# Kernel optimization log

Hardware: AMD Instinct MI355X
Metric: run time of the kernel (lower is better)

The kernel has to match this reference:

```python
import jax, jax.numpy as jnp
import numpy as np

N, E, H, NH = 50000, 500000, 128, 8
DH = H // NH


def _bn(x, g, b, eps=1e-5):
    # BatchNorm1d in training mode: biased batch statistics over the node dim
    mu = x.mean(0)
    var = ((x - mu) ** 2).mean(0)
    return (x - mu) * jax.lax.rsqrt(var + eps) * g + b


def setup_inputs() -> dict:
    key = jax.random.key(0)
    ks = jax.random.split(key, 16)
    W = lambda k, shape: jax.random.normal(k, shape, jnp.float32) * 0.02
    return {
        "h": jax.random.normal(ks[0], (N, H), jnp.float32),
        "eattr": jax.random.normal(ks[1], (E, H), jnp.float32),
        "src": jax.random.randint(ks[2], (E,), 0, N, jnp.int32),
        "dst": jax.random.randint(ks[3], (E,), 0, N, jnp.int32),
        "gin_w1": W(ks[4], (H, H)), "gin_b1": jnp.zeros((H,), jnp.float32),
        "gin_w2": W(ks[5], (H, H)), "gin_b2": jnp.zeros((H,), jnp.float32),
        "wq": W(ks[6], (H, H)), "bq": jnp.zeros((H,), jnp.float32),
        "wk": W(ks[7], (H, H)), "bk": jnp.zeros((H,), jnp.float32),
        "wv": W(ks[8], (H, H)), "bv": jnp.zeros((H,), jnp.float32),
        "nl_g": jnp.ones((H,), jnp.float32), "nl_b": jnp.zeros((H,), jnp.float32),
        "na_g": jnp.ones((H,), jnp.float32), "na_b": jnp.zeros((H,), jnp.float32),
        "no_g": jnp.ones((H,), jnp.float32), "no_b": jnp.zeros((H,), jnp.float32),
        "ffn1_w": W(ks[9], (2 * H, H)), "ffn1_b": jnp.zeros((2 * H,), jnp.float32),
        "ffn2_w": W(ks[10], (H, 2 * H)), "ffn2_b": jnp.zeros((H,), jnp.float32),
    }


def reference(h, eattr, src, dst, gin_w1, gin_b1, gin_w2, gin_b2,
              wq, bq, wk, bk, wv, bv, nl_g, nl_b, na_g, na_b, no_g, no_b,
              ffn1_w, ffn1_b, ffn2_w, ffn2_b):
    h_in = h

    # --- local model: GINEConv (eps=0) ---
    msg = jax.nn.relu(h[src] + eattr)                       # [E,H]
    agg = jax.ops.segment_sum(msg, dst, num_segments=N)     # [N,H]
    z = h + agg                                             # (1+eps)*h + sum
    h_local = jax.nn.relu(z @ gin_w1.T + gin_b1) @ gin_w2.T + gin_b2
    h_local = _bn(h_in + h_local, nl_g, nl_b)               # dropout=0

    # --- global attention: SparseMHA over the edge list ---
    scale = DH ** -0.5
    q = ((h @ wq.T + bq) * scale).reshape(N, NH, DH)
    k = (h @ wk.T + bk).reshape(N, NH, DH)
    v = (h @ wv.T + bv).reshape(N, NH, DH)
    s = jnp.einsum("ehd,ehd->eh", q[src], k[dst])           # per-edge scores [E,NH]
    m = jax.ops.segment_max(s, src, num_segments=N)         # row-wise max [N,NH]
    p = jnp.exp(s - m[src])
    denom = jax.ops.segment_sum(p, src, num_segments=N)     # [N,NH]
    attn = p / denom[src]                                   # sparse row softmax [E,NH]
    out = jax.ops.segment_sum(attn[:, :, None] * v[dst], src, num_segments=N)
    h_attn = out.reshape(N, H)
    h_attn = _bn(h_in + h_attn, na_g, na_b)

    # --- combine + FFN + out norm ---
    hc = h_local + h_attn
    hc = hc + (jax.nn.relu(hc @ ffn1_w.T + ffn1_b) @ ffn2_w.T + ffn2_b)
    hc = _bn(hc, no_g, no_b)
    return (hc, eattr)
```

## Files before the change

### kernel.cpp

```cpp
#include <hip/hip_runtime.h>

#define NN 50000
#define NE 500000
#define HD 128

typedef unsigned short ushort_t;
typedef __bf16 bf16x8 __attribute__((ext_vector_type(8)));
typedef float f32x4 __attribute__((ext_vector_type(4)));
typedef float f32x2 __attribute__((ext_vector_type(2)));

static __device__ __forceinline__ unsigned short f2bf(float f) {
  unsigned int u = __float_as_uint(f);
  unsigned int r = (u + 0x7fffu + ((u >> 16) & 1u)) >> 16;
  return (unsigned short)r;
}
static __device__ __forceinline__ float2 ldbf2(const unsigned short* p) {
  unsigned int u = *reinterpret_cast<const unsigned int*>(p);
  return make_float2(__uint_as_float(u << 16), __uint_as_float(u & 0xffff0000u));
}

__global__ __launch_bounds__(256) void hist_kernel(const int* __restrict__ src, const int* __restrict__ dst,
                                                   int* __restrict__ deg_src, int* __restrict__ deg_dst, int E) {
  int e = blockIdx.x * 256 + threadIdx.x;
  if (e < E) {
    atomicAdd(&deg_dst[dst[e]], 1);
    atomicAdd(&deg_src[src[e]], 1);
  }
}

__global__ __launch_bounds__(1024) void scan_kernel(const int* __restrict__ deg_dst, const int* __restrict__ deg_src,
                                                    int* __restrict__ off_dst, int* __restrict__ cur_dst,
                                                    int* __restrict__ off_src, int* __restrict__ cur_src, int N) {
  const int* deg = blockIdx.x ? deg_src : deg_dst;
  int* off = blockIdx.x ? off_src : off_dst;
  int* cur = blockIdx.x ? cur_src : cur_dst;
  const int CH = (N + 1023) / 1024;
  int t = threadIdx.x;
  int base = t * CH;
  int sum = 0;
  for (int i = 0; i < CH; ++i) { int idx = base + i; if (idx < N) sum += deg[idx]; }
  __shared__ int ls[1024];
  ls[t] = sum;
  __syncthreads();
  for (int o = 1; o < 1024; o <<= 1) {
    int u = (t >= o) ? ls[t - o] : 0;
    __syncthreads();
    ls[t] += u;
    __syncthreads();
  }
  int run = ls[t] - sum;
  for (int i = 0; i < CH; ++i) {
    int idx = base + i;
    if (idx < N) { off[idx] = run; cur[idx] = run; run += deg[idx]; }
  }
  if (t == 1023) off[N] = ls[1023];
}

__global__ __launch_bounds__(256) void scatter_kernel(const int* __restrict__ src, const int* __restrict__ dst,
                                                      int* __restrict__ cur_src, int* __restrict__ cur_dst,
                                                      int* __restrict__ adj_src, int2* __restrict__ pair_dst, int E) {
  int e = blockIdx.x * 256 + threadIdx.x;
  if (e < E) {
    int s = src[e], d = dst[e];
    int p = atomicAdd(&cur_dst[d], 1); pair_dst[p] = make_int2(e, s);
    int q = atomicAdd(&cur_src[s], 1); adj_src[q] = d;
  }
}

__global__ __launch_bounds__(256) void hconv_kernel(const float* __restrict__ h, ushort_t* __restrict__ hb, int total4) {
  int i = blockIdx.x * 256 + threadIdx.x;
  if (i >= total4) return;
  float4 v = reinterpret_cast<const float4*>(h)[i];
  ushort4 u = { f2bf(v.x), f2bf(v.y), f2bf(v.z), f2bf(v.w) };
  reinterpret_cast<ushort4*>(hb)[i] = u;
}

template <int K, int OUTC, int MODE>
__global__ __launch_bounds__(256) void gemm_kernel(const ushort_t* __restrict__ A, const float* __restrict__ W,
                                                   const float* __restrict__ bias, const float* __restrict__ resid,
                                                   void* __restrict__ out, float scale, int nrows) {
  constexpr int KP = K + 8;
  __shared__ __align__(16) ushort_t wlds[OUTC * KP];
  constexpr int NLOAD = OUTC * K / 4;
  for (int idx = threadIdx.x; idx < NLOAD; idx += 256) {
    int r = idx / (K / 4), c4 = idx % (K / 4);
    float4 wv = reinterpret_cast<const float4*>(W)[idx];
    ushort_t* d = &wlds[r * KP + c4 * 4];
    d[0] = f2bf(wv.x); d[1] = f2bf(wv.y); d[2] = f2bf(wv.z); d[3] = f2bf(wv.w);
  }
  __syncthreads();
  const int wave = threadIdx.x >> 6, lane = threadIdx.x & 63;
  const int row0 = (blockIdx.x * 4 + wave) * 16;
  if (row0 >= nrows) return;
  const int m = lane & 15, quad = lane >> 4;
  bf16x8 afrag[K / 32];
  {
    const ushort_t* ar = A + (size_t)(row0 + m) * K + quad * 8;
#pragma unroll
    for (int kk = 0; kk < K / 32; ++kk)
      afrag[kk] = *reinterpret_cast<const bf16x8*>(ar + kk * 32);
  }
  f32x4 acc[OUTC / 16] = {};
#pragma unroll
  for (int c = 0; c < OUTC / 16; ++c) {
    const ushort_t* wr = &wlds[(c * 16 + m) * KP + quad * 8];
#pragma unroll
    for (int kk = 0; kk < K / 32; ++kk) {
      bf16x8 bfrag = *reinterpret_cast<const bf16x8*>(wr + kk * 32);
      acc[c] = __builtin_amdgcn_mfma_f32_16x16x32_bf16(afrag[kk], bfrag, acc[c], 0, 0, 0);
    }
  }
#pragma unroll
  for (int c = 0; c < OUTC / 16; ++c) {
    int col = c * 16 + m;
    float bv = bias[col];
#pragma unroll
    for (int r = 0; r < 4; ++r) {
      int grow = row0 + quad * 4 + r;
      float val = (acc[c][r] + bv) * scale;
      if constexpr (MODE & 1) val = fmaxf(val, 0.0f);
      if constexpr (MODE & 2) val += resid[(size_t)grow * OUTC + col];
      if constexpr (MODE & 4) ((ushort_t*)out)[(size_t)grow * OUTC + col] = f2bf(val);
      else ((float*)out)[(size_t)grow * OUTC + col] = val;
    }
  }
}

__global__ __launch_bounds__(256) void agg_kernel(const float* __restrict__ h, const float* __restrict__ eattr,
                                                  const int* __restrict__ off_dst, const int2* __restrict__ pair_dst,
                                                  float* __restrict__ out_eattr, ushort_t* __restrict__ z_bf, int N) {
  int wave = threadIdx.x >> 6, lane = threadIdx.x & 63;
  int n = blockIdx.x * 4 + wave;
  if (n >= N) return;
  int c2 = lane * 2;
  float a0 = 0.f, a1 = 0.f;
  int beg = off_dst[n], end = off_dst[n + 1];
  int i = beg;
  int mainend = beg + ((end - beg) & ~3);
  if (i < mainend) {
    int2 p0 = pair_dst[i], p1 = pair_dst[i + 1], p2 = pair_dst[i + 2], p3 = pair_dst[i + 3];
    for (;;) {
      f32x2 ea0 = __builtin_nontemporal_load(reinterpret_cast<const f32x2*>(eattr + (size_t)p0.x * HD + c2));
      f32x2 ea1 = __builtin_nontemporal_load(reinterpret_cast<const f32x2*>(eattr + (size_t)p1.x * HD + c2));
      f32x2 ea2 = __builtin_nontemporal_load(reinterpret_cast<const f32x2*>(eattr + (size_t)p2.x * HD + c2));
      f32x2 ea3 = __builtin_nontemporal_load(reinterpret_cast<const f32x2*>(eattr + (size_t)p3.x * HD + c2));
      f32x2 hs0 = *reinterpret_cast<const f32x2*>(h + (size_t)p0.y * HD + c2);
      f32x2 hs1 = *reinterpret_cast<const f32x2*>(h + (size_t)p1.y * HD + c2);
      f32x2 hs2 = *reinterpret_cast<const f32x2*>(h + (size_t)p2.y * HD + c2);
      f32x2 hs3 = *reinterpret_cast<const f32x2*>(h + (size_t)p3.y * HD + c2);
      int ni = i + 4;
      int pi = (ni < mainend) ? ni : beg;
      int2 q0 = pair_dst[pi], q1 = pair_dst[pi + 1], q2 = pair_dst[pi + 2], q3 = pair_dst[pi + 3];
      __builtin_nontemporal_store(ea0, reinterpret_cast<f32x2*>(out_eattr + (size_t)p0.x * HD + c2));
      __builtin_nontemporal_store(ea1, reinterpret_cast<f32x2*>(out_eattr + (size_t)p1.x * HD + c2));
      __builtin_nontemporal_store(ea2, reinterpret_cast<f32x2*>(out_eattr + (size_t)p2.x * HD + c2));
      __builtin_nontemporal_store(ea3, reinterpret_cast<f32x2*>(out_eattr + (size_t)p3.x * HD + c2));
      a0 += (fmaxf(hs0.x + ea0.x, 0.f) + fmaxf(hs1.x + ea1.x, 0.f)) +
            (fmaxf(hs2.x + ea2.x, 0.f) + fmaxf(hs3.x + ea3.x, 0.f));
      a1 += (fmaxf(hs0.y + ea0.y, 0.f) + fmaxf(hs1.y + ea1.y, 0.f)) +
            (fmaxf(hs2.y + ea2.y, 0.f) + fmaxf(hs3.y + ea3.y, 0.f));
      p0 = q0; p1 = q1; p2 = q2; p3 = q3;
      i = ni;
      if (i >= mainend) break;
    }
  }
  for (; i < end; ++i) {
    int2 p = pair_dst[i];
    f32x2 ea = __builtin_nontemporal_load(reinterpret_cast<const f32x2*>(eattr + (size_t)p.x * HD + c2));
    f32x2 hs = *reinterpret_cast<const f32x2*>(h + (size_t)p.y * HD + c2);
    __builtin_nontemporal_store(ea, reinterpret_cast<f32x2*>(out_eattr + (size_t)p.x * HD + c2));
    a0 += fmaxf(hs.x + ea.x, 0.f);
    a1 += fmaxf(hs.y + ea.y, 0.f);
  }
  float2 hn = *reinterpret_cast<const float2*>(h + (size_t)n * HD + c2);
  ushort2 u = { f2bf(hn.x + a0), f2bf(hn.y + a1) };
  *reinterpret_cast<ushort2*>(z_bf + (size_t)n * HD + c2) = u;
}

__global__ __launch_bounds__(256) void attn_kernel(const ushort_t* __restrict__ qb, const ushort_t* __restrict__ kb,
                                                   const ushort_t* __restrict__ vb, const int* __restrict__ off_src,
                                                   const int* __restrict__ adj_src,
                                                   const float* __restrict__ h, float* __restrict__ X2, int N) {
  int wave = threadIdx.x >> 6, lane = threadIdx.x & 63;
  int n = blockIdx.x * 4 + wave;
  if (n >= N) return;
  int c2 = lane * 2;
  float2 qv = ldbf2(qb + (size_t)n * HD + c2);
  float m = -__builtin_inff(), l = 0.f, a0 = 0.f, a1 = 0.f;
  int beg = off_src[n], end = off_src[n + 1];
  int i = beg;
  int mainend = beg + ((end - beg) & ~3);
  if (i < mainend) {
    int d0 = adj_src[i], d1 = adj_src[i + 1], d2 = adj_src[i + 2], d3 = adj_src[i + 3];
    for (;;) {
      float2 k0 = ldbf2(kb + (size_t)d0 * HD + c2);
      float2 k1 = ldbf2(kb + (size_t)d1 * HD + c2);
      float2 k2 = ldbf2(kb + (size_t)d2 * HD + c2);
      float2 k3 = ldbf2(kb + (size_t)d3 * HD + c2);
      float2 v0 = ldbf2(vb + (size_t)d0 * HD + c2);
      float2 v1 = ldbf2(vb + (size_t)d1 * HD + c2);
      float2 v2 = ldbf2(vb + (size_t)d2 * HD + c2);
      float2 v3 = ldbf2(vb + (size_t)d3 * HD + c2);
      int ni = i + 4;
      int pi = (ni < mainend) ? ni : beg;
      int e0 = adj_src[pi], e1 = adj_src[pi + 1], e2 = adj_src[pi + 2], e3 = adj_src[pi + 3];
      float s0 = qv.x * k0.x + qv.y * k0.y;
      float s1 = qv.x * k1.x + qv.y * k1.y;
      float s2 = qv.x * k2.x + qv.y * k2.y;
      float s3 = qv.x * k3.x + qv.y * k3.y;
      s0 += __shfl_xor(s0, 1, 64); s0 += __shfl_xor(s0, 2, 64); s0 += __shfl_xor(s0, 4, 64);
      s1 += __shfl_xor(s1, 1, 64); s1 += __shfl_xor(s1, 2, 64); s1 += __shfl_xor(s1, 4, 64);
      s2 += __shfl_xor(s2, 1, 64); s2 += __shfl_xor(s2, 2, 64); s2 += __shfl_xor(s2, 4, 64);
      s3 += __shfl_xor(s3, 1, 64); s3 += __shfl_xor(s3, 2, 64); s3 += __shfl_xor(s3, 4, 64);
      float smax = fmaxf(fmaxf(s0, s1), fmaxf(s2, s3));
      float nm = fmaxf(m, smax);
      float al = __expf(m - nm);
      float p0 = __expf(s0 - nm), p1 = __expf(s1 - nm), p2 = __expf(s2 - nm), p3 = __expf(s3 - nm);
      l = l * al + ((p0 + p1) + (p2 + p3));
      a0 = a0 * al + ((p0 * v0.x + p1 * v1.x) + (p2 * v2.x + p3 * v3.x));
      a1 = a1 * al + ((p0 * v0.y + p1 * v1.y) + (p2 * v2.y + p3 * v3.y));
      m = nm;
      d0 = e0; d1 = e1; d2 = e2; d3 = e3;
      i = ni;
      if (i >= mainend) break;
    }
  }
  for (; i < end; ++i) {
    int d = adj_src[i];
    float2 kd = ldbf2(kb + (size_t)d * HD + c2);
    float s = qv.x * kd.x + qv.y * kd.y;
    s += __shfl_xor(s, 1, 64);
    s += __shfl_xor(s, 2, 64);
    s += __shfl_xor(s, 4, 64);
    float2 vd = ldbf2(vb + (size_t)d * HD + c2);
    float nm = fmaxf(m, s);
    float al = __expf(m - nm);
    float p = __expf(s - nm);
    l = l * al + p;
    a0 = a0 * al + p * vd.x;
    a1 = a1 * al + p * vd.y;
    m = nm;
  }
  float inv = (end > beg) ? 1.0f / l : 0.f;
  size_t base = (size_t)n * HD + c2;
  float2 hv = *reinterpret_cast<const float2*>(h + base);
  float2 o = make_float2(hv.x + a0 * inv, hv.y + a1 * inv);
  *reinterpret_cast<float2*>(X2 + base) = o;
}

__global__ __launch_bounds__(256) void stats_kernel(const float* __restrict__ X, float* __restrict__ sums,
                                                    float* __restrict__ sumsq, int N) {
  int col = threadIdx.x & 127, half = threadIdx.x >> 7;
  float s = 0.f, s2 = 0.f;
  for (int r = blockIdx.x * 2 + half; r < N; r += gridDim.x * 2) {
    float v = X[(size_t)r * HD + col];
    s += v;
    s2 += v * v;
  }
  __shared__ float ls[256], ls2[256];
  ls[threadIdx.x] = s;
  ls2[threadIdx.x] = s2;
  __syncthreads();
  if (half == 0) {
    s += ls[threadIdx.x + 128];
    s2 += ls2[threadIdx.x + 128];
    atomicAdd(&sums[col], s);
    atomicAdd(&sumsq[col], s2);
  }
}

__global__ void coeff_kernel(const float* __restrict__ sums, const float* __restrict__ sumsq,
                             const float* __restrict__ g, const float* __restrict__ b, float* __restrict__ ab, int N) {
  int c = threadIdx.x;
  float inv_n = 1.0f / (float)N;
  float mu = sums[c] * inv_n;
  float var = sumsq[c] * inv_n - mu * mu;
  float a = g[c] * rsqrtf(var + 1e-5f);
  ab[c] = a;
  ab[128 + c] = b[c] - mu * a;
}

__global__ __launch_bounds__(256) void combine_kernel(const float* __restrict__ X1, const float* __restrict__ X2,
                                                      const float* __restrict__ ab1, const float* __restrict__ ab2,
                                                      float* __restrict__ hc_f, ushort_t* __restrict__ hc_b, int total4) {
  int i = blockIdx.x * 256 + threadIdx.x;
  if (i >= total4) return;
  float4 x1 = reinterpret_cast<const float4*>(X1)[i];
  float4 x2 = reinterpret_cast<const float4*>(X2)[i];
  int c = (i * 4) & 127;
  float4 r;
  r.x = x1.x * ab1[c + 0] + ab1[128 + c + 0] + x2.x * ab2[c + 0] + ab2[128 + c + 0];
  r.y = x1.y * ab1[c + 1] + ab1[128 + c + 1] + x2.y * ab2[c + 1] + ab2[128 + c + 1];
  r.z = x1.z * ab1[c + 2] + ab1[128 + c + 2] + x2.z * ab2[c + 2] + ab2[128 + c + 2];
  r.w = x1.w * ab1[c + 3] + ab1[128 + c + 3] + x2.w * ab2[c + 3] + ab2[128 + c + 3];
  reinterpret_cast<float4*>(hc_f)[i] = r;
  ushort4 u = { f2bf(r.x), f2bf(r.y), f2bf(r.z), f2bf(r.w) };
  reinterpret_cast<ushort4*>(hc_b)[i] = u;
}

__global__ __launch_bounds__(256) void final_kernel(const float* __restrict__ X3, const float* __restrict__ ab,
                                                    float* __restrict__ out, int total4) {
  int i = blockIdx.x * 256 + threadIdx.x;
  if (i >= total4) return;
  float4 x = reinterpret_cast<const float4*>(X3)[i];
  int c = (i * 4) & 127;
  float4 r;
  r.x = x.x * ab[c + 0] + ab[128 + c + 0];
  r.y = x.y * ab[c + 1] + ab[128 + c + 1];
  r.z = x.z * ab[c + 2] + ab[128 + c + 2];
  r.w = x.w * ab[c + 3] + ab[128 + c + 3];
  reinterpret_cast<float4*>(out)[i] = r;
}

extern "C" void kernel_launch(void* const* d_in, const int* in_sizes, int n_in,
                              void* d_out, int out_size, void* d_ws, size_t ws_size,
                              hipStream_t stream) {
  const float* h = (const float*)d_in[0];
  const float* eattr = (const float*)d_in[1];
  const int* src = (const int*)d_in[2];
  const int* dst = (const int*)d_in[3];
  const float* gin_w1 = (const float*)d_in[4];
  const float* gin_b1 = (const float*)d_in[5];
  const float* gin_w2 = (const float*)d_in[6];
  const float* gin_b2 = (const float*)d_in[7];
  const float* wq = (const float*)d_in[8];
  const float* bq = (const float*)d_in[9];
  const float* wk = (const float*)d_in[10];
  const float* bk = (const float*)d_in[11];
  const float* wv = (const float*)d_in[12];
  const float* bv = (const float*)d_in[13];
  const float* nl_g = (const float*)d_in[14];
  const float* nl_b = (const float*)d_in[15];
  const float* na_g = (const float*)d_in[16];
  const float* na_b = (const float*)d_in[17];
  const float* no_g = (const float*)d_in[18];
  const float* no_b = (const float*)d_in[19];
  const float* ffn1_w = (const float*)d_in[20];
  const float* ffn1_b = (const float*)d_in[21];
  const float* ffn2_w = (const float*)d_in[22];
  const float* ffn2_b = (const float*)d_in[23];

  const int N = NN, E = NE;
  char* ws = (char*)d_ws;
  size_t off = 0;
  auto alloc = [&](size_t bytes) -> void* {
    void* p = ws + off;
    off += (bytes + 255) & ~(size_t)255;
    return p;
  };

  ushort_t* h_bf = (ushort_t*)alloc((size_t)N * HD * 2);
  ushort_t* q_bf = (ushort_t*)alloc((size_t)N * HD * 2);
  ushort_t* k_bf = (ushort_t*)alloc((size_t)N * HD * 2);
  ushort_t* v_bf = (ushort_t*)alloc((size_t)N * HD * 2);
  ushort_t* z_bf = (ushort_t*)alloc((size_t)N * HD * 2);
  ushort_t* mid1 = (ushort_t*)alloc((size_t)N * HD * 2);
  ushort_t* hc_bf = (ushort_t*)alloc((size_t)N * HD * 2);
  ushort_t* mid2 = (ushort_t*)alloc((size_t)N * 256 * 2);
  float* X1 = (float*)alloc((size_t)N * HD * 4);
  float* X2 = (float*)alloc((size_t)N * HD * 4);
  float* X3 = (float*)alloc((size_t)N * HD * 4);
  float* hc_f = (float*)alloc((size_t)N * HD * 4);
  int* deg_dst = (int*)alloc((size_t)N * 4);
  int* deg_src = (int*)alloc((size_t)N * 4);
  float* stats = (float*)alloc(6 * 128 * 4);
  size_t zero_bytes = (size_t)((char*)(stats + 6 * 128) - (char*)deg_dst);
  int* off_dst = (int*)alloc((size_t)(N + 1) * 4);
  int* off_src = (int*)alloc((size_t)(N + 1) * 4);
  int* cur_dst = (int*)alloc((size_t)N * 4);
  int* cur_src = (int*)alloc((size_t)N * 4);
  int2* pair_dst = (int2*)alloc((size_t)E * 8);
  int* adj_src = (int*)alloc((size_t)E * 4);
  float* ab1 = (float*)alloc(256 * 4);
  float* ab2 = (float*)alloc(256 * 4);
  float* ab3 = (float*)alloc(256 * 4);

  float* sums1 = stats, *sq1 = stats + 128;
  float* sums2 = stats + 256, *sq2 = stats + 384;
  float* sums3 = stats + 512, *sq3 = stats + 640;

  float* out_hc = (float*)d_out;
  float* out_eattr = (float*)d_out + (size_t)N * HD;

  hipMemsetAsync(deg_dst, 0, zero_bytes, stream);

  const int egrid = (E + 255) / 256;
  hist_kernel<<<egrid, 256, 0, stream>>>(src, dst, deg_src, deg_dst, E);
  scan_kernel<<<2, 1024, 0, stream>>>(deg_dst, deg_src, off_dst, cur_dst, off_src, cur_src, N);
  scatter_kernel<<<egrid, 256, 0, stream>>>(src, dst, cur_src, cur_dst, adj_src, pair_dst, E);

  const int total4 = N * HD / 4;
  const int cgrid = (total4 + 255) / 256;
  hconv_kernel<<<cgrid, 256, 0, stream>>>(h, h_bf, total4);

  const int ggrid = (N / 16 + 3) / 4;
  const float scale = 0.25f;
  gemm_kernel<128, 128, 4><<<ggrid, 256, 0, stream>>>(h_bf, wq, bq, nullptr, q_bf, scale, N);
  gemm_kernel<128, 128, 4><<<ggrid, 256, 0, stream>>>(h_bf, wk, bk, nullptr, k_bf, 1.0f, N);
  gemm_kernel<128, 128, 4><<<ggrid, 256, 0, stream>>>(h_bf, wv, bv, nullptr, v_bf, 1.0f, N);

  agg_kernel<<<N / 4, 256, 0, stream>>>(h, eattr, off_dst, pair_dst, out_eattr, z_bf, N);
  gemm_kernel<128, 128, 5><<<ggrid, 256, 0, stream>>>(z_bf, gin_w1, gin_b1, nullptr, mid1, 1.0f, N);
  gemm_kernel<128, 128, 2><<<ggrid, 256, 0, stream>>>(mid1, gin_w2, gin_b2, h, X1, 1.0f, N);

  attn_kernel<<<N / 4, 256, 0, stream>>>(q_bf, k_bf, v_bf, off_src, adj_src, h, X2, N);

  stats_kernel<<<256, 256, 0, stream>>>(X1, sums1, sq1, N);
  stats_kernel<<<256, 256, 0, stream>>>(X2, sums2, sq2, N);
  coeff_kernel<<<1, 128, 0, stream>>>(sums1, sq1, nl_g, nl_b, ab1, N);
  coeff_kernel<<<1, 128, 0, stream>>>(sums2, sq2, na_g, na_b, ab2, N);
  combine_kernel<<<cgrid, 256, 0, stream>>>(X1, X2, ab1, ab2, hc_f, hc_bf, total4);

  gemm_kernel<128, 256, 5><<<ggrid, 256, 0, stream>>>(hc_bf, ffn1_w, ffn1_b, nullptr, mid2, 1.0f, N);
  gemm_kernel<256, 128, 2><<<ggrid, 256, 0, stream>>>(mid2, ffn2_w, ffn2_b, hc_f, X3, 1.0f, N);

  stats_kernel<<<256, 256, 0, stream>>>(X3, sums3, sq3, N);
  coeff_kernel<<<1, 128, 0, stream>>>(sums3, sq3, no_g, no_b, ab3, N);
  final_kernel<<<cgrid, 256, 0, stream>>>(X3, ab3, out_hc, total4);
}
```

Before: 1.003 ms.

## Fuse QKV projections, bf16 conversion, and BN stats into GEMM kernels

Replaces the separate h-to-bf16 conversion and three Q/K/V GEMM launches with one qkv kernel that converts fp32 h on load and reuses the A fragments across the three weight matrices. The GEMM kernel now processes 32 rows per wave, sharing each B fragment across two MFMA tiles. It can also accumulate BatchNorm sums and sums of squares in its epilogue, which removes two stats passes and the bf16 copy of hc. The cost is more registers per wave (two accumulator sets, up to 256 columns wide), which can lower occupancy, plus extra atomics on the stats buffers.

```diff
diff --git a/kernel.cpp b/kernel.cpp
--- a/kernel.cpp
+++ b/kernel.cpp
@@ -67,18 +67,11 @@
   }
 }
 
-__global__ __launch_bounds__(256) void hconv_kernel(const float* __restrict__ h, ushort_t* __restrict__ hb, int total4) {
-  int i = blockIdx.x * 256 + threadIdx.x;
-  if (i >= total4) return;
-  float4 v = reinterpret_cast<const float4*>(h)[i];
-  ushort4 u = { f2bf(v.x), f2bf(v.y), f2bf(v.z), f2bf(v.w) };
-  reinterpret_cast<ushort4*>(hb)[i] = u;
-}
-
 template <int K, int OUTC, int MODE>
-__global__ __launch_bounds__(256) void gemm_kernel(const ushort_t* __restrict__ A, const float* __restrict__ W,
+__global__ __launch_bounds__(256) void gemm_kernel(const void* __restrict__ Ap, const float* __restrict__ W,
                                                    const float* __restrict__ bias, const float* __restrict__ resid,
-                                                   void* __restrict__ out, float scale, int nrows) {
+                                                   void* __restrict__ out, float* __restrict__ stats,
+                                                   float scale, int nrows) {
   constexpr int KP = K + 8;
   __shared__ __align__(16) ushort_t wlds[OUTC * KP];
   constexpr int NLOAD = OUTC * K / 4;
@@ -90,39 +83,159 @@
   }
   __syncthreads();
   const int wave = threadIdx.x >> 6, lane = threadIdx.x & 63;
-  const int row0 = (blockIdx.x * 4 + wave) * 16;
-  if (row0 >= nrows) return;
   const int m = lane & 15, quad = lane >> 4;
-  bf16x8 afrag[K / 32];
-  {
-    const ushort_t* ar = A + (size_t)(row0 + m) * K + quad * 8;
-#pragma unroll
-    for (int kk = 0; kk < K / 32; ++kk)
-      afrag[kk] = *reinterpret_cast<const bf16x8*>(ar + kk * 32);
-  }
-  f32x4 acc[OUTC / 16] = {};
+  const int row0 = (blockIdx.x * 4 + wave) * 32;
+  const bool vt[2] = { row0 < nrows, row0 + 16 < nrows };
+  bf16x8 afrag[2][K / 32];
+#pragma unroll
+  for (int t = 0; t < 2; ++t) {
+    int rowt = vt[t] ? (row0 + t * 16 + m) : 0;
+    if constexpr (MODE & 16) {
+      const float* ar = (const float*)Ap + (size_t)rowt * K + quad * 8;
+#pragma unroll
+      for (int kk = 0; kk < K / 32; ++kk) {
+        float4 x = *reinterpret_cast<const float4*>(ar + kk * 32);
+        float4 y = *reinterpret_cast<const float4*>(ar + kk * 32 + 4);
+        union { bf16x8 v8; ushort_t u[8]; } pk;
+        pk.u[0] = f2bf(x.x); pk.u[1] = f2bf(x.y); pk.u[2] = f2bf(x.z); pk.u[3] = f2bf(x.w);
+        pk.u[4] = f2bf(y.x); pk.u[5] = f2bf(y.y); pk.u[6] = f2bf(y.z); pk.u[7] = f2bf(y.w);
+        afrag[t][kk] = pk.v8;
+      }
+    } else {
+      const ushort_t* ar = (const ushort_t*)Ap + (size_t)rowt * K + quad * 8;
+#pragma unroll
+      for (int kk = 0; kk < K / 32; ++kk)
+        afrag[t][kk] = *reinterpret_cast<const bf16x8*>(ar + kk * 32);
+    }
+  }
+  f32x4 acc[2][OUTC / 16] = {};
 #pragma unroll
   for (int c = 0; c < OUTC / 16; ++c) {
     const ushort_t* wr = &wlds[(c * 16 + m) * KP + quad * 8];
 #pragma unroll
     for (int kk = 0; kk < K / 32; ++kk) {
       bf16x8 bfrag = *reinterpret_cast<const bf16x8*>(wr + kk * 32);
-      acc[c] = __builtin_amdgcn_mfma_f32_16x16x32_bf16(afrag[kk], bfrag, acc[c], 0, 0, 0);
-    }
-  }
-#pragma unroll
-  for (int c = 0; c < OUTC / 16; ++c) {
-    int col = c * 16 + m;
-    float bv = bias[col];
-#pragma unroll
-    for (int r = 0; r < 4; ++r) {
-      int grow = row0 + quad * 4 + r;
-      float val = (acc[c][r] + bv) * scale;
-      if constexpr (MODE & 1) val = fmaxf(val, 0.0f);
-      if constexpr (MODE & 2) val += resid[(size_t)grow * OUTC + col];
-      if constexpr (MODE & 4) ((ushort_t*)out)[(size_t)grow * OUTC + col] = f2bf(val);
-      else ((float*)out)[(size_t)grow * OUTC + col] = val;
-    }
+      acc[0][c] = __builtin_amdgcn_mfma_f32_16x16x32_bf16(afrag[0][kk], bfrag, acc[0][c], 0, 0, 0);
+      acc[1][c] = __builtin_amdgcn_mfma_f32_16x16x32_bf16(afrag[1][kk], bfrag, acc[1][c], 0, 0, 0);
+    }
+  }
+  float s1r[OUTC / 16] = {}, s2r[OUTC / 16] = {};
+#pragma unroll
+  for (int t = 0; t < 2; ++t) {
+    if (vt[t]) {
+#pragma unroll
+      for (int c = 0; c < OUTC / 16; ++c) {
+        int col = c * 16 + m;
+        float bv = bias[col];
+#pragma unroll
+        for (int r = 0; r < 4; ++r) {
+          int grow = row0 + t * 16 + quad * 4 + r;
+          float val = (acc[t][c][r] + bv) * scale;
+          if constexpr (MODE & 1) val = fmaxf(val, 0.0f);
+          if constexpr (MODE & 2) val += resid[(size_t)grow * OUTC + col];
+          if constexpr (MODE & 4) ((ushort_t*)out)[(size_t)grow * OUTC + col] = f2bf(val);
+          else ((float*)out)[(size_t)grow * OUTC + col] = val;
+          if constexpr (MODE & 8) { s1r[c] += val; s2r[c] += val * val; }
+        }
+      }
+    }
+  }
+  if constexpr (MODE & 8) {
+#pragma unroll
+    for (int c = 0; c < OUTC / 16; ++c) {
+      s1r[c] += __shfl_xor(s1r[c], 16, 64); s1r[c] += __shfl_xor(s1r[c], 32, 64);
+      s2r[c] += __shfl_xor(s2r[c], 16, 64); s2r[c] += __shfl_xor(s2r[c], 32, 64);
+    }
+    __shared__ float sred[2][4][OUTC / 16][16];
+    if (lane < 16) {
+#pragma unroll
+      for (int c = 0; c < OUTC / 16; ++c) {
+        sred[0][wave][c][lane] = s1r[c];
+        sred[1][wave][c][lane] = s2r[c];
+      }
+    }
+    __syncthreads();
+    int tid = threadIdx.x;
+    if (tid < 2 * OUTC) {
+      int which = tid >= OUTC ? 1 : 0;
+      int col = tid - which * OUTC;
+      float tot = sred[which][0][col >> 4][col & 15] + sred[which][1][col >> 4][col & 15] +
+                  sred[which][2][col >> 4][col & 15] + sred[which][3][col >> 4][col & 15];
+      atomicAdd(&stats[which * OUTC + col], tot);
+    }
+  }
+}
+
+__global__ __launch_bounds__(256) void qkv_kernel(const float* __restrict__ h,
+                                                  const float* __restrict__ wq, const float* __restrict__ bq,
+                                                  const float* __restrict__ wk, const float* __restrict__ bk,
+                                                  const float* __restrict__ wv, const float* __restrict__ bv,
+                                                  ushort_t* __restrict__ qb, ushort_t* __restrict__ kb,
+                                                  ushort_t* __restrict__ vb, int nrows) {
+  constexpr int K = HD, OUTC = HD, KP = K + 8;
+  __shared__ __align__(16) ushort_t wlds[OUTC * KP];
+  const int wave = threadIdx.x >> 6, lane = threadIdx.x & 63;
+  const int m = lane & 15, quad = lane >> 4;
+  const int row0 = (blockIdx.x * 4 + wave) * 32;
+  const bool vt[2] = { row0 < nrows, row0 + 16 < nrows };
+  bf16x8 afrag[2][K / 32];
+#pragma unroll
+  for (int t = 0; t < 2; ++t) {
+    int rowt = vt[t] ? (row0 + t * 16 + m) : 0;
+    const float* ar = h + (size_t)rowt * K + quad * 8;
+#pragma unroll
+    for (int kk = 0; kk < K / 32; ++kk) {
+      float4 x = *reinterpret_cast<const float4*>(ar + kk * 32);
+      float4 y = *reinterpret_cast<const float4*>(ar + kk * 32 + 4);
+      union { bf16x8 v8; ushort_t u[8]; } pk;
+      pk.u[0] = f2bf(x.x); pk.u[1] = f2bf(x.y); pk.u[2] = f2bf(x.z); pk.u[3] = f2bf(x.w);
+      pk.u[4] = f2bf(y.x); pk.u[5] = f2bf(y.y); pk.u[6] = f2bf(y.z); pk.u[7] = f2bf(y.w);
+      afrag[t][kk] = pk.v8;
+    }
+  }
+  const float* Ws[3] = { wq, wk, wv };
+  const float* Bs[3] = { bq, bk, bv };
+  ushort_t* Os[3] = { qb, kb, vb };
+  for (int w = 0; w < 3; ++w) {
+    const float* W = Ws[w];
+    constexpr int NLOAD = OUTC * K / 4;
+    for (int idx = threadIdx.x; idx < NLOAD; idx += 256) {
+      int r = idx / (K / 4), c4 = idx % (K / 4);
+      float4 wv4 = reinterpret_cast<const float4*>(W)[idx];
+      ushort_t* d = &wlds[r * KP + c4 * 4];
+      d[0] = f2bf(wv4.x); d[1] = f2bf(wv4.y); d[2] = f2bf(wv4.z); d[3] = f2bf(wv4.w);
+    }
+    __syncthreads();
+    f32x4 acc[2][OUTC / 16] = {};
+#pragma unroll
+    for (int c = 0; c < OUTC / 16; ++c) {
+      const ushort_t* wr = &wlds[(c * 16 + m) * KP + quad * 8];
+#pragma unroll
+      for (int kk = 0; kk < K / 32; ++kk) {
+        bf16x8 bfrag = *reinterpret_cast<const bf16x8*>(wr + kk * 32);
+        acc[0][c] = __builtin_amdgcn_mfma_f32_16x16x32_bf16(afrag[0][kk], bfrag, acc[0][c], 0, 0, 0);
+        acc[1][c] = __builtin_amdgcn_mfma_f32_16x16x32_bf16(afrag[1][kk], bfrag, acc[1][c], 0, 0, 0);
+      }
+    }
+    float scl = (w == 0) ? 0.25f : 1.0f;
+    ushort_t* O = Os[w];
+    const float* B = Bs[w];
+#pragma unroll
+    for (int t = 0; t < 2; ++t) {
+      if (vt[t]) {
+#pragma unroll
+        for (int c = 0; c < OUTC / 16; ++c) {
+          int col = c * 16 + m;
+          float bv = B[col];
+#pragma unroll
+          for (int r = 0; r < 4; ++r) {
+            int grow = row0 + t * 16 + quad * 4 + r;
+            O[(size_t)grow * OUTC + col] = f2bf((acc[t][c][r] + bv) * scl);
+          }
+        }
+      }
+    }
+    __syncthreads();
   }
 }
 
@@ -282,7 +395,7 @@
 
 __global__ __launch_bounds__(256) void combine_kernel(const float* __restrict__ X1, const float* __restrict__ X2,
                                                       const float* __restrict__ ab1, const float* __restrict__ ab2,
-                                                      float* __restrict__ hc_f, ushort_t* __restrict__ hc_b, int total4) {
+                                                      float* __restrict__ hc_f, int total4) {
   int i = blockIdx.x * 256 + threadIdx.x;
   if (i >= total4) return;
   float4 x1 = reinterpret_cast<const float4*>(X1)[i];
@@ -294,8 +407,6 @@
   r.z = x1.z * ab1[c + 2] + ab1[128 + c + 2] + x2.z * ab2[c + 2] + ab2[128 + c + 2];
   r.w = x1.w * ab1[c + 3] + ab1[128 + c + 3] + x2.w * ab2[c + 3] + ab2[128 + c + 3];
   reinterpret_cast<float4*>(hc_f)[i] = r;
-  ushort4 u = { f2bf(r.x), f2bf(r.y), f2bf(r.z), f2bf(r.w) };
-  reinterpret_cast<ushort4*>(hc_b)[i] = u;
 }
 
 __global__ __launch_bounds__(256) void final_kernel(const float* __restrict__ X3, const float* __restrict__ ab,
@@ -349,13 +460,11 @@
     return p;
   };
 
-  ushort_t* h_bf = (ushort_t*)alloc((size_t)N * HD * 2);
   ushort_t* q_bf = (ushort_t*)alloc((size_t)N * HD * 2);
   ushort_t* k_bf = (ushort_t*)alloc((size_t)N * HD * 2);
   ushort_t* v_bf = (ushort_t*)alloc((size_t)N * HD * 2);
   ushort_t* z_bf = (ushort_t*)alloc((size_t)N * HD * 2);
   ushort_t* mid1 = (ushort_t*)alloc((size_t)N * HD * 2);
-  ushort_t* hc_bf = (ushort_t*)alloc((size_t)N * HD * 2);
   ushort_t* mid2 = (ushort_t*)alloc((size_t)N * 256 * 2);
   float* X1 = (float*)alloc((size_t)N * HD * 4);
   float* X2 = (float*)alloc((size_t)N * HD * 4);
@@ -375,9 +484,10 @@
   float* ab2 = (float*)alloc(256 * 4);
   float* ab3 = (float*)alloc(256 * 4);
 
-  float* sums1 = stats, *sq1 = stats + 128;
-  float* sums2 = stats + 256, *sq2 = stats + 384;
-  float* sums3 = stats + 512, *sq3 = stats + 640;
+  float* sums1 = stats;
+  float* sums2 = stats + 256;
+  float* sums3 = stats + 512;
+  float* sq2 = stats + 384;
 
   float* out_hc = (float*)d_out;
   float* out_eattr = (float*)d_out + (size_t)N * HD;
@@ -391,30 +501,24 @@
 
   const int total4 = N * HD / 4;
   const int cgrid = (total4 + 255) / 256;
-  hconv_kernel<<<cgrid, 256, 0, stream>>>(h, h_bf, total4);
-
-  const int ggrid = (N / 16 + 3) / 4;
-  const float scale = 0.25f;
-  gemm_kernel<128, 128, 4><<<ggrid, 256, 0, stream>>>(h_bf, wq, bq, nullptr, q_bf, scale, N);
-  gemm_kernel<128, 128, 4><<<ggrid, 256, 0, stream>>>(h_bf, wk, bk, nullptr, k_bf, 1.0f, N);
-  gemm_kernel<128, 128, 4><<<ggrid, 256, 0, stream>>>(h_bf, wv, bv, nullptr, v_bf, 1.0f, N);
+  const int g2 = (N + 127) / 128;
+
+  qkv_kernel<<<g2, 256, 0, stream>>>(h, wq, bq, wk, bk, wv, bv, q_bf, k_bf, v_bf, N);
 
   agg_kernel<<<N / 4, 256, 0, stream>>>(h, eattr, off_dst, pair_dst, out_eattr, z_bf, N);
-  gemm_kernel<128, 128, 5><<<ggrid, 256, 0, stream>>>(z_bf, gin_w1, gin_b1, nullptr, mid1, 1.0f, N);
-  gemm_kernel<128, 128, 2><<<ggrid, 256, 0, stream>>>(mid1, gin_w2, gin_b2, h, X1, 1.0f, N);
+  gemm_kernel<128, 128, 5><<<g2, 256, 0, stream>>>(z_bf, gin_w1, gin_b1, nullptr, mid1, nullptr, 1.0f, N);
+  gemm_kernel<128, 128, 10><<<g2, 256, 0, stream>>>(mid1, gin_w2, gin_b2, h, X1, sums1, 1.0f, N);
 
   attn_kernel<<<N / 4, 256, 0, stream>>>(q_bf, k_bf, v_bf, off_src, adj_src, h, X2, N);
 
-  stats_kernel<<<256, 256, 0, stream>>>(X1, sums1, sq1, N);
   stats_kernel<<<256, 256, 0, stream>>>(X2, sums2, sq2, N);
-  coeff_kernel<<<1, 128, 0, stream>>>(sums1, sq1, nl_g, nl_b, ab1, N);
-  coeff_kernel<<<1, 128, 0, stream>>>(sums2, sq2, na_g, na_b, ab2, N);
-  combine_kernel<<<cgrid, 256, 0, stream>>>(X1, X2, ab1, ab2, hc_f, hc_bf, total4);
-
-  gemm_kernel<128, 256, 5><<<ggrid, 256, 0, stream>>>(hc_bf, ffn1_w, ffn1_b, nullptr, mid2, 1.0f, N);
-  gemm_kernel<256, 128, 2><<<ggrid, 256, 0, stream>>>(mid2, ffn2_w, ffn2_b, hc_f, X3, 1.0f, N);
-
-  stats_kernel<<<256, 256, 0, stream>>>(X3, sums3, sq3, N);
-  coeff_kernel<<<1, 128, 0, stream>>>(sums3, sq3, no_g, no_b, ab3, N);
+  coeff_kernel<<<1, 128, 0, stream>>>(sums1, sums1 + 128, nl_g, nl_b, ab1, N);
+  coeff_kernel<<<1, 128, 0, stream>>>(sums2, sums2 + 128, na_g, na_b, ab2, N);
+  combine_kernel<<<cgrid, 256, 0, stream>>>(X1, X2, ab1, ab2, hc_f, total4);
+
+  gemm_kernel<128, 256, 21><<<g2, 256, 0, stream>>>(hc_f, ffn1_w, ffn1_b, nullptr, mid2, nullptr, 1.0f, N);
+  gemm_kernel<256, 128, 10><<<g2, 256, 0, stream>>>(mid2, ffn2_w, ffn2_b, hc_f, X3, sums3, 1.0f, N);
+
+  coeff_kernel<<<1, 128, 0, stream>>>(sums3, sums3 + 128, no_g, no_b, ab3, N);
   final_kernel<<<cgrid, 256, 0, stream>>>(X3, ab3, out_hc, total4);
 }
```

After: 961.5 us. 4.1% less time.
